# Performance work log

Hardware: AMD Instinct MI355X
Metric: run time of the kernel (lower is better)

The kernel has to match this reference:

```python
import jax, jax.numpy as jnp
import numpy as np

N_NODES = 40000


def gcn_conv(x, W, b, src, dst, deg_inv_sqrt, n_nodes):
    # x: [N, Din], W: [Din, Dout]
    h = x @ W  # [N, Dout]
    norm = deg_inv_sqrt[src] * deg_inv_sqrt[dst]  # [E'] (edges incl. self-loops)
    msg = h[src] * norm[:, None]  # gather + scale: [E', Dout]
    out = jax.ops.segment_sum(msg, dst, num_segments=n_nodes)  # scatter-add
    return out + b


def setup_inputs() -> dict:
    key = jax.random.key(0)
    k1, k2, k3, k4, k5, k6 = jax.random.split(key, 6)
    x = jax.random.normal(k1, (N_NODES, 512), dtype=jnp.float32)
    edge_index = jax.random.randint(k2, (2, 640000), 0, N_NODES, dtype=jnp.int64)
    W1 = jax.random.normal(k3, (512, 256), dtype=jnp.float32) * (1.0 / np.sqrt(512))
    b1 = jax.random.normal(k4, (256,), dtype=jnp.float32) * 0.01
    W2 = jax.random.normal(k5, (256, 47), dtype=jnp.float32) * (1.0 / np.sqrt(256))
    b2 = jax.random.normal(k6, (47,), dtype=jnp.float32) * 0.01
    return {"x": x, "edge_index": edge_index, "W1": W1, "b1": b1, "W2": W2, "b2": b2}


def reference(x, edge_index, W1, b1, W2, b2):
    n = x.shape[0]
    loops = jnp.arange(n, dtype=edge_index.dtype)
    # add self-loops (PyG GCNConv default)
    src = jnp.concatenate([edge_index[0], loops])
    dst = jnp.concatenate([edge_index[1], loops])
    # symmetric normalization: deg over A + I (unit edge weights)
    deg = jax.ops.segment_sum(jnp.ones_like(dst, dtype=x.dtype), dst, num_segments=n)
    deg_inv_sqrt = jnp.where(deg > 0, jax.lax.rsqrt(jnp.maximum(deg, 1e-12)), 0.0)

    h = gcn_conv(x, W1, b1, src, dst, deg_inv_sqrt, n)
    h = jax.nn.relu(h)
    # dropout is identity in eval mode (training=False)
    h = gcn_conv(h, W2, b2, src, dst, deg_inv_sqrt, n)
    return jax.nn.log_softmax(h, axis=1)
```

## Files before the change

kernel.cpp:

```cpp
#include <hip/hip_runtime.h>


typedef _Float16 f16;
typedef _Float16 f16x8 __attribute__((ext_vector_type(8)));
typedef float f32x4 __attribute__((ext_vector_type(4)));

#define N_NODES 40000
#define N_EDGES 640000
#define D_IN 512
#define D_HID 256
#define D_OUT 47
#define D_OUT_PAD 48


__global__ void k_degree(const int* __restrict__ eidx, int* __restrict__ deg) {
    int e = blockIdx.x * blockDim.x + threadIdx.x;
    if (e < N_EDGES) atomicAdd(&deg[eidx[N_EDGES + e]], 1);
}

__global__ __launch_bounds__(1024) void k_scan(const int* __restrict__ deg,
                                               int* __restrict__ rowptr,
                                               float* __restrict__ dinv) {
    __shared__ int wsum[16];
    const int S = 40;
    int t = threadIdx.x;
    int lane = t & 63;
    int wid = t >> 6;
    int base = t * S;
    bool live = (base < N_NODES);

    int v[S];
    int tot = 0;
#pragma unroll
    for (int i = 0; i < S / 4; ++i) {
        int4 q = make_int4(0, 0, 0, 0);
        if (live) q = *(const int4*)(deg + base + i * 4);
        v[i * 4 + 0] = q.x; v[i * 4 + 1] = q.y;
        v[i * 4 + 2] = q.z; v[i * 4 + 3] = q.w;
        tot += q.x + q.y + q.z + q.w;
    }
    int inc = tot;
#pragma unroll
    for (int off = 1; off < 64; off <<= 1) {
        int n = __shfl_up(inc, off);
        if (lane >= off) inc += n;
    }
    if (lane == 63) wsum[wid] = inc;
    __syncthreads();
    if (t < 16) {
        int wv = wsum[t];
        int winc = wv;
#pragma unroll
        for (int off = 1; off < 16; off <<= 1) {
            int n = __shfl_up(winc, off);
            if (t >= off) winc += n;
        }
        wsum[t] = winc - wv;
    }
    __syncthreads();
    int acc = wsum[wid] + (inc - tot);
#pragma unroll
    for (int i = 0; i < S / 4; ++i) {
        int4 r; float4 f;
        r.x = acc; f.x = rsqrtf((float)(v[i * 4 + 0] + 1)); acc += v[i * 4 + 0];
        r.y = acc; f.y = rsqrtf((float)(v[i * 4 + 1] + 1)); acc += v[i * 4 + 1];
        r.z = acc; f.z = rsqrtf((float)(v[i * 4 + 2] + 1)); acc += v[i * 4 + 2];
        r.w = acc; f.w = rsqrtf((float)(v[i * 4 + 3] + 1)); acc += v[i * 4 + 3];
        if (live) {
            *(int4*)(rowptr + base + i * 4) = r;
            *(float4*)(dinv + base + i * 4) = f;
        }
    }
    if (t == 0) rowptr[N_NODES] = N_EDGES;
}

__global__ void k_fill(const int* __restrict__ eidx, const int* __restrict__ rowptr,
                       int* __restrict__ cursor, int* __restrict__ col) {
    int e = blockIdx.x * blockDim.x + threadIdx.x;
    if (e < N_EDGES) {
        int s = eidx[e];
        int d = eidx[N_EDGES + e];
        int pos = atomicAdd(&cursor[d], 1);
        col[rowptr[d] + pos] = s;
    }
}


__global__ void k_pack_w1(const float* __restrict__ W, f16* __restrict__ Wp) {
    int u = blockIdx.x * blockDim.x + threadIdx.x;
    if (u >= 16 * 16 * 64) return;
    int l = u & 63;
    int nf = (u >> 6) & 15;
    int kt = u >> 10;
    int k0 = kt * 32 + (l >> 4) * 8;
    int c = nf * 16 + (l & 15);
    f16x8 o;
#pragma unroll
    for (int j = 0; j < 8; ++j) o[j] = (f16)W[(size_t)(k0 + j) * D_HID + c];
    *(f16x8*)(Wp + (size_t)u * 8) = o;
}

__global__ void k_pack_w2(const float* __restrict__ W, f16* __restrict__ Wp) {
    int u = blockIdx.x * blockDim.x + threadIdx.x;
    if (u >= 8 * 3 * 64) return;
    int l = u & 63;
    int nf = (u / 64) % 3;
    int kt = u / 192;
    int k0 = kt * 32 + (l >> 4) * 8;
    int c = nf * 16 + (l & 15);
    f16x8 o;
#pragma unroll
    for (int j = 0; j < 8; ++j)
        o[j] = (c < D_OUT) ? (f16)W[(size_t)(k0 + j) * D_OUT + c] : (f16)0.0f;
    *(f16x8*)(Wp + (size_t)u * 8) = o;
}


__global__ __launch_bounds__(256) void k_gemm1(const float* __restrict__ X,
                                               const f16* __restrict__ Bp,
                                               f16* __restrict__ C) {
    int wid = threadIdx.x >> 6;
    int lane = threadIdx.x & 63;
    int rowBase = blockIdx.x * 64;
    int nf0 = wid * 4;
    int r_ = lane & 15, q_ = lane >> 4;

    f32x4 acc[4][4];
#pragma unroll
    for (int mi = 0; mi < 4; ++mi)
#pragma unroll
        for (int ni = 0; ni < 4; ++ni) acc[mi][ni] = (f32x4)(0.0f);

    for (int kt = 0; kt < 16; ++kt) {
        int k0 = kt * 32 + q_ * 8;
        f16x8 a[4], b[4];
#pragma unroll
        for (int mi = 0; mi < 4; ++mi) {
            const float4* p = (const float4*)(X + (size_t)(rowBase + mi * 16 + r_) * D_IN + k0);
            float4 lo = p[0], hi = p[1];
            f16x8 t;
            t[0] = (f16)lo.x; t[1] = (f16)lo.y; t[2] = (f16)lo.z; t[3] = (f16)lo.w;
            t[4] = (f16)hi.x; t[5] = (f16)hi.y; t[6] = (f16)hi.z; t[7] = (f16)hi.w;
            a[mi] = t;
        }
#pragma unroll
        for (int ni = 0; ni < 4; ++ni)
            b[ni] = *(const f16x8*)(Bp + ((size_t)(kt * 16 + nf0 + ni) * 64 + lane) * 8);
#pragma unroll
        for (int mi = 0; mi < 4; ++mi)
#pragma unroll
            for (int ni = 0; ni < 4; ++ni)
                acc[mi][ni] = __builtin_amdgcn_mfma_f32_16x16x32_f16(a[mi], b[ni], acc[mi][ni], 0, 0, 0);
    }

    int r0 = (lane >> 4) * 4;
    int c0 = lane & 15;
#pragma unroll
    for (int mi = 0; mi < 4; ++mi)
#pragma unroll
        for (int ni = 0; ni < 4; ++ni)
#pragma unroll
            for (int r = 0; r < 4; ++r) {
                int row = rowBase + mi * 16 + r0 + r;
                C[(size_t)row * D_HID + (nf0 + ni) * 16 + c0] = (f16)acc[mi][ni][r];
            }
}


__global__ __launch_bounds__(256) void k_gemm2(const f16* __restrict__ Ap,
                                               const f16* __restrict__ Bp,
                                               f16* __restrict__ C) {
    int wid = threadIdx.x >> 6;
    int lane = threadIdx.x & 63;
    int rowTile = blockIdx.x * 4 + wid;
    int rowBase = rowTile * 64;
    if (rowBase >= N_NODES) return;

    f32x4 acc[4][3];
#pragma unroll
    for (int mi = 0; mi < 4; ++mi)
#pragma unroll
        for (int ni = 0; ni < 3; ++ni) acc[mi][ni] = (f32x4)(0.0f);

    int m16b = rowTile * 4;
    for (int kt = 0; kt < 8; ++kt) {
        f16x8 a[4], b[3];
#pragma unroll
        for (int mi = 0; mi < 4; ++mi)
            a[mi] = *(const f16x8*)(Ap + ((size_t)((m16b + mi) * 8 + kt) * 64 + lane) * 8);
#pragma unroll
        for (int ni = 0; ni < 3; ++ni)
            b[ni] = *(const f16x8*)(Bp + ((size_t)(kt * 3 + ni) * 64 + lane) * 8);
#pragma unroll
        for (int mi = 0; mi < 4; ++mi)
#pragma unroll
            for (int ni = 0; ni < 3; ++ni)
                acc[mi][ni] = __builtin_amdgcn_mfma_f32_16x16x32_f16(a[mi], b[ni], acc[mi][ni], 0, 0, 0);
    }

    int r0 = (lane >> 4) * 4;
    int c0 = lane & 15;
#pragma unroll
    for (int mi = 0; mi < 4; ++mi)
#pragma unroll
        for (int ni = 0; ni < 3; ++ni)
#pragma unroll
            for (int r = 0; r < 4; ++r) {
                int row = rowBase + mi * 16 + r0 + r;
                C[(size_t)row * D_OUT_PAD + ni * 16 + c0] = (f16)acc[mi][ni][r];
            }
}


__global__ __launch_bounds__(256) void k_agg1(const f16* __restrict__ h1,
                                              const int* __restrict__ rowptr,
                                              const int* __restrict__ col,
                                              const float* __restrict__ dinv,
                                              const float* __restrict__ b1,
                                              f16* __restrict__ hp) {
    int node = blockIdx.x * 4 + (threadIdx.x >> 6);
    int lane = threadIdx.x & 63;
    int half = lane >> 5;
    int hl = lane & 31;
    float di = dinv[node];

    f16x8 selfv = *(const f16x8*)(h1 + (size_t)node * D_HID + hl * 8);

    float a[8];
#pragma unroll
    for (int j = 0; j < 8; ++j) a[j] = 0.0f;

    int e0 = rowptr[node], e1 = rowptr[node + 1];
    for (int base = e0; base < e1; base += 64) {
        int nn = min(64, e1 - base);
        int sidx = 0; float wv = 0.0f;
        if (lane < nn) {
            int s = col[base + lane];
            sidx = s;
            wv = dinv[s] * di;
        }
        int t = half;
        for (; t + 2 < nn; t += 4) {
            int s0 = __shfl(sidx, t), s1 = __shfl(sidx, t + 2);
            float w0 = __shfl(wv, t), w1 = __shfl(wv, t + 2);
            f16x8 u0 = *(const f16x8*)(h1 + (size_t)s0 * D_HID + hl * 8);
            f16x8 u1 = *(const f16x8*)(h1 + (size_t)s1 * D_HID + hl * 8);
#pragma unroll
            for (int j = 0; j < 8; ++j)
                a[j] += (float)u0[j] * w0 + (float)u1[j] * w1;
        }
        if (t < nn) {
            int s0 = __shfl(sidx, t);
            float w0 = __shfl(wv, t);
            f16x8 u0 = *(const f16x8*)(h1 + (size_t)s0 * D_HID + hl * 8);
#pragma unroll
            for (int j = 0; j < 8; ++j) a[j] += (float)u0[j] * w0;
        }
    }

#pragma unroll
    for (int j = 0; j < 8; ++j) a[j] += __shfl_xor(a[j], 32);

    float wself = di * di;
    float4 b_lo = *(const float4*)(b1 + hl * 8);
    float4 b_hi = *(const float4*)(b1 + hl * 8 + 4);
    f16x8 o;
    o[0] = (f16)fmaxf(a[0] + (float)selfv[0] * wself + b_lo.x, 0.0f);
    o[1] = (f16)fmaxf(a[1] + (float)selfv[1] * wself + b_lo.y, 0.0f);
    o[2] = (f16)fmaxf(a[2] + (float)selfv[2] * wself + b_lo.z, 0.0f);
    o[3] = (f16)fmaxf(a[3] + (float)selfv[3] * wself + b_lo.w, 0.0f);
    o[4] = (f16)fmaxf(a[4] + (float)selfv[4] * wself + b_hi.x, 0.0f);
    o[5] = (f16)fmaxf(a[5] + (float)selfv[5] * wself + b_hi.y, 0.0f);
    o[6] = (f16)fmaxf(a[6] + (float)selfv[6] * wself + b_hi.z, 0.0f);
    o[7] = (f16)fmaxf(a[7] + (float)selfv[7] * wself + b_hi.w, 0.0f);

    if (half == 0) {
        size_t idx = ((size_t)(node >> 4) * 8 + (hl >> 2)) * 512 + (hl & 3) * 128 + (node & 15) * 8;
        *(f16x8*)(hp + idx) = o;
    }
}


__global__ __launch_bounds__(256) void k_agg2(const f16* __restrict__ g,
                                              const int* __restrict__ rowptr,
                                              const int* __restrict__ col,
                                              const float* __restrict__ dinv,
                                              const float* __restrict__ b2,
                                              float* __restrict__ out) {
    int node = blockIdx.x * 4 + (threadIdx.x >> 6);
    int lane = threadIdx.x & 63;
    float di = dinv[node];
    bool act = lane < D_OUT_PAD;
    float acc = act ? (float)g[(size_t)node * D_OUT_PAD + lane] * di * di : 0.0f;

    int e0 = rowptr[node], e1 = rowptr[node + 1];
    for (int base = e0; base < e1; base += 64) {
        int nn = min(64, e1 - base);
        int sidx = 0; float wv = 0.0f;
        if (lane < nn) {
            int s = col[base + lane];
            sidx = s;
            wv = dinv[s] * di;
        }
        int k = 0;
        for (; k + 4 <= nn; k += 4) {
            int s0 = __shfl(sidx, k), s1 = __shfl(sidx, k + 1);
            int s2 = __shfl(sidx, k + 2), s3 = __shfl(sidx, k + 3);
            float w0 = __shfl(wv, k), w1 = __shfl(wv, k + 1);
            float w2 = __shfl(wv, k + 2), w3 = __shfl(wv, k + 3);
            if (act) {
                float u0 = (float)g[(size_t)s0 * D_OUT_PAD + lane];
                float u1 = (float)g[(size_t)s1 * D_OUT_PAD + lane];
                float u2 = (float)g[(size_t)s2 * D_OUT_PAD + lane];
                float u3 = (float)g[(size_t)s3 * D_OUT_PAD + lane];
                acc += u0 * w0 + u1 * w1 + u2 * w2 + u3 * w3;
            }
        }
        for (; k < nn; ++k) {
            int s0 = __shfl(sidx, k);
            float w0 = __shfl(wv, k);
            if (act) acc += (float)g[(size_t)s0 * D_OUT_PAD + lane] * w0;
        }
    }

    float z = (lane < D_OUT) ? acc + b2[lane] : -3.0e38f;
    float mx = z;
#pragma unroll
    for (int off = 32; off >= 1; off >>= 1) mx = fmaxf(mx, __shfl_xor(mx, off));
    float ex = (lane < D_OUT) ? expf(z - mx) : 0.0f;
    float sum = ex;
#pragma unroll
    for (int off = 32; off >= 1; off >>= 1) sum += __shfl_xor(sum, off);
    if (lane < D_OUT) out[(size_t)node * D_OUT + lane] = z - mx - logf(sum);
}


extern "C" void kernel_launch(void* const* d_in, const int* in_sizes, int n_in,
                              void* d_out, int out_size, void* d_ws, size_t ws_size,
                              hipStream_t stream) {
    const float* x  = (const float*)d_in[0];
    const int*   ei = (const int*)d_in[1];
    const float* W1 = (const float*)d_in[2];
    const float* b1 = (const float*)d_in[3];
    const float* W2 = (const float*)d_in[4];
    const float* b2 = (const float*)d_in[5];
    float* out = (float*)d_out;

    char* ws = (char*)d_ws;
    int*   degi   = (int*)(ws + 0);
    int*   cursor = (int*)(ws + 160000);
    float* dinv   = (float*)(ws + 320000);
    int*   rowptr = (int*)(ws + 480000);
    int*   col    = (int*)(ws + 640256);
    f16*   w1p    = (f16*)(ws + 3200256);
    f16*   w2p    = (f16*)(ws + 3462400);
    f16*   h1     = (f16*)(ws + 3486976);
    f16*   hpk    = (f16*)(ws + 23966976);
    f16*   g      = (f16*)(ws + 44446976);

    hipMemsetAsync(d_ws, 0, 320000, stream);

    k_degree<<<2500, 256, 0, stream>>>(ei, degi);
    k_scan<<<1, 1024, 0, stream>>>(degi, rowptr, dinv);
    k_fill<<<2500, 256, 0, stream>>>(ei, rowptr, cursor, col);

    k_pack_w1<<<64, 256, 0, stream>>>(W1, w1p);
    k_pack_w2<<<6, 256, 0, stream>>>(W2, w2p);

    k_gemm1<<<625, 256, 0, stream>>>(x, w1p, h1);
    k_agg1<<<10000, 256, 0, stream>>>(h1, rowptr, col, dinv, b1, hpk);
    k_gemm2<<<157, 256, 0, stream>>>(hpk, w2p, g);
    k_agg2<<<10000, 256, 0, stream>>>(g, rowptr, col, dinv, b2, out);
}
```

Baseline: 224.9 us.

## Retile gemm1 to 32x64 warp tiles with double-buffered register prefetch

Each block of gemm1 now covers a 64-row by 128-column tile instead of 64 rows by 256 columns, and each warp owns 32 rows by 64 columns. The grid doubles to 1250 blocks. The k-loop is fully unrolled with two register sets, so loads for the next k-step are issued before the MFMAs of the current step to hide global-load latency. The cost is that every X row is now read twice from global (once per column half) and register pressure goes up from the double buffering.

```diff
diff --git a/kernel.cpp b/kernel.cpp
--- a/kernel.cpp
+++ b/kernel.cpp
@@ -116,53 +116,86 @@
 }
 
 
+#define G1_LOADA(areg, kt_)                                                  \
+    {                                                                        \
+        int k0 = (kt_) * 32 + q_ * 8;                                        \
+        const float4* p0 = (const float4*)(xrow0 + k0);                      \
+        const float4* p1 = (const float4*)(xrow1 + k0);                      \
+        float4 lo0 = p0[0], hi0 = p0[1], lo1 = p1[0], hi1 = p1[1];           \
+        f16x8 t0, t1;                                                        \
+        t0[0] = (f16)lo0.x; t0[1] = (f16)lo0.y; t0[2] = (f16)lo0.z;          \
+        t0[3] = (f16)lo0.w; t0[4] = (f16)hi0.x; t0[5] = (f16)hi0.y;          \
+        t0[6] = (f16)hi0.z; t0[7] = (f16)hi0.w;                              \
+        t1[0] = (f16)lo1.x; t1[1] = (f16)lo1.y; t1[2] = (f16)lo1.z;          \
+        t1[3] = (f16)lo1.w; t1[4] = (f16)hi1.x; t1[5] = (f16)hi1.y;          \
+        t1[6] = (f16)hi1.z; t1[7] = (f16)hi1.w;                              \
+        areg##0 = t0; areg##1 = t1;                                          \
+    }
+
+#define G1_LOADB(breg, kt_)                                                  \
+    {                                                                        \
+        const f16* bp = Bp + ((size_t)((kt_) * 16 + nf0) * 64 + lane) * 8;   \
+        breg##0 = *(const f16x8*)(bp);                                       \
+        breg##1 = *(const f16x8*)(bp + 512);                                 \
+        breg##2 = *(const f16x8*)(bp + 1024);                                \
+        breg##3 = *(const f16x8*)(bp + 1536);                                \
+    }
+
+#define G1_MFMA(areg, breg)                                                  \
+    acc00 = __builtin_amdgcn_mfma_f32_16x16x32_f16(areg##0, breg##0, acc00, 0, 0, 0); \
+    acc01 = __builtin_amdgcn_mfma_f32_16x16x32_f16(areg##0, breg##1, acc01, 0, 0, 0); \
+    acc02 = __builtin_amdgcn_mfma_f32_16x16x32_f16(areg##0, breg##2, acc02, 0, 0, 0); \
+    acc03 = __builtin_amdgcn_mfma_f32_16x16x32_f16(areg##0, breg##3, acc03, 0, 0, 0); \
+    acc10 = __builtin_amdgcn_mfma_f32_16x16x32_f16(areg##1, breg##0, acc10, 0, 0, 0); \
+    acc11 = __builtin_amdgcn_mfma_f32_16x16x32_f16(areg##1, breg##1, acc11, 0, 0, 0); \
+    acc12 = __builtin_amdgcn_mfma_f32_16x16x32_f16(areg##1, breg##2, acc12, 0, 0, 0); \
+    acc13 = __builtin_amdgcn_mfma_f32_16x16x32_f16(areg##1, breg##3, acc13, 0, 0, 0);
+
 __global__ __launch_bounds__(256) void k_gemm1(const float* __restrict__ X,
                                                const f16* __restrict__ Bp,
                                                f16* __restrict__ C) {
     int wid = threadIdx.x >> 6;
     int lane = threadIdx.x & 63;
-    int rowBase = blockIdx.x * 64;
-    int nf0 = wid * 4;
+    int rb = blockIdx.x >> 1;
+    int cb = blockIdx.x & 1;
+    int rowBase = rb * 64 + (wid >> 1) * 32;
+    int nf0 = cb * 8 + (wid & 1) * 4;
     int r_ = lane & 15, q_ = lane >> 4;
 
-    f32x4 acc[4][4];
-#pragma unroll
-    for (int mi = 0; mi < 4; ++mi)
-#pragma unroll
-        for (int ni = 0; ni < 4; ++ni) acc[mi][ni] = (f32x4)(0.0f);
-
-    for (int kt = 0; kt < 16; ++kt) {
-        int k0 = kt * 32 + q_ * 8;
-        f16x8 a[4], b[4];
-#pragma unroll
-        for (int mi = 0; mi < 4; ++mi) {
-            const float4* p = (const float4*)(X + (size_t)(rowBase + mi * 16 + r_) * D_IN + k0);
-            float4 lo = p[0], hi = p[1];
-            f16x8 t;
-            t[0] = (f16)lo.x; t[1] = (f16)lo.y; t[2] = (f16)lo.z; t[3] = (f16)lo.w;
-            t[4] = (f16)hi.x; t[5] = (f16)hi.y; t[6] = (f16)hi.z; t[7] = (f16)hi.w;
-            a[mi] = t;
-        }
-#pragma unroll
-        for (int ni = 0; ni < 4; ++ni)
-            b[ni] = *(const f16x8*)(Bp + ((size_t)(kt * 16 + nf0 + ni) * 64 + lane) * 8);
-#pragma unroll
-        for (int mi = 0; mi < 4; ++mi)
-#pragma unroll
-            for (int ni = 0; ni < 4; ++ni)
-                acc[mi][ni] = __builtin_amdgcn_mfma_f32_16x16x32_f16(a[mi], b[ni], acc[mi][ni], 0, 0, 0);
+    const float* xrow0 = X + (size_t)(rowBase + r_) * D_IN;
+    const float* xrow1 = X + (size_t)(rowBase + 16 + r_) * D_IN;
+
+    f32x4 acc00 = (f32x4)(0.0f), acc01 = (f32x4)(0.0f), acc02 = (f32x4)(0.0f), acc03 = (f32x4)(0.0f);
+    f32x4 acc10 = (f32x4)(0.0f), acc11 = (f32x4)(0.0f), acc12 = (f32x4)(0.0f), acc13 = (f32x4)(0.0f);
+
+    f16x8 pA0, pA1, pB0, pB1, pB2, pB3;
+    f16x8 qA0, qA1, qB0, qB1, qB2, qB3;
+
+    G1_LOADA(pA, 0)
+    G1_LOADB(pB, 0)
+#pragma unroll
+    for (int kt = 0; kt < 16; kt += 2) {
+        G1_LOADA(qA, kt + 1)
+        G1_LOADB(qB, kt + 1)
+        G1_MFMA(pA, pB)
+        if (kt + 2 < 16) {
+            G1_LOADA(pA, kt + 2)
+            G1_LOADB(pB, kt + 2)
+        }
+        G1_MFMA(qA, qB)
     }
 
     int r0 = (lane >> 4) * 4;
     int c0 = lane & 15;
-#pragma unroll
-    for (int mi = 0; mi < 4; ++mi)
+    f32x4 accs[2][4] = {{acc00, acc01, acc02, acc03}, {acc10, acc11, acc12, acc13}};
+#pragma unroll
+    for (int mi = 0; mi < 2; ++mi)
 #pragma unroll
         for (int ni = 0; ni < 4; ++ni)
 #pragma unroll
             for (int r = 0; r < 4; ++r) {
                 int row = rowBase + mi * 16 + r0 + r;
-                C[(size_t)row * D_HID + (nf0 + ni) * 16 + c0] = (f16)acc[mi][ni][r];
+                C[(size_t)row * D_HID + (nf0 + ni) * 16 + c0] = (f16)accs[mi][ni][r];
             }
 }
 
@@ -367,7 +400,7 @@
     k_pack_w1<<<64, 256, 0, stream>>>(W1, w1p);
     k_pack_w2<<<6, 256, 0, stream>>>(W2, w2p);
 
-    k_gemm1<<<625, 256, 0, stream>>>(x, w1p, h1);
+    k_gemm1<<<1250, 256, 0, stream>>>(x, w1p, h1);
     k_agg1<<<10000, 256, 0, stream>>>(h1, rowptr, col, dinv, b1, hpk);
     k_gemm2<<<157, 256, 0, stream>>>(hpk, w2p, g);
     k_agg2<<<10000, 256, 0, stream>>>(g, rowptr, col, dinv, b2, out);
```

Result: no change. 221.8 us (-1.3%).

## Stage converted X tile in LDS and split GEMM1 across eight waves

Applied to the files above, without the earlier changes.

GEMM1 now loads the block's 64x512 fp32 X tile once with coalesced float4 reads, converts it to fp16 and stores it in padded shared memory. The MFMA loop then reads A fragments from LDS. Block size goes from 4 to 8 waves, with each wave covering 2 output column tiles instead of 4, so the X rows are not read redundantly by every wave from global memory. In exchange it uses about 66 KB of LDS per block, which limits how many blocks fit per CU, and adds a full-tile sync before any compute starts.

```diff
diff --git a/kernel.cpp b/kernel.cpp
--- a/kernel.cpp
+++ b/kernel.cpp
@@ -3,6 +3,7 @@
 
 typedef _Float16 f16;
 typedef _Float16 f16x8 __attribute__((ext_vector_type(8)));
+typedef _Float16 f16x4 __attribute__((ext_vector_type(4)));
 typedef float f32x4 __attribute__((ext_vector_type(4)));
 
 #define N_NODES 40000
@@ -116,49 +117,58 @@
 }
 
 
-__global__ __launch_bounds__(256) void k_gemm1(const float* __restrict__ X,
+__global__ __launch_bounds__(512) void k_gemm1(const float* __restrict__ X,
                                                const f16* __restrict__ Bp,
                                                f16* __restrict__ C) {
-    int wid = threadIdx.x >> 6;
-    int lane = threadIdx.x & 63;
+    __shared__ f16 As[64][520];
+    int t = threadIdx.x;
+    int lane = t & 63;
+    int wid = t >> 6;
     int rowBase = blockIdx.x * 64;
-    int nf0 = wid * 4;
+
+#pragma unroll
+    for (int it = 0; it < 16; ++it) {
+        int idx = it * 512 + t;
+        int row = idx >> 7;
+        int c4 = idx & 127;
+        float4 v = *(const float4*)(X + (size_t)(rowBase + row) * D_IN + c4 * 4);
+        f16x4 o;
+        o[0] = (f16)v.x; o[1] = (f16)v.y; o[2] = (f16)v.z; o[3] = (f16)v.w;
+        *(f16x4*)(&As[row][c4 * 4]) = o;
+    }
+    __syncthreads();
+
+    int nf0 = wid * 2;
     int r_ = lane & 15, q_ = lane >> 4;
 
-    f32x4 acc[4][4];
+    f32x4 acc[4][2];
 #pragma unroll
     for (int mi = 0; mi < 4; ++mi)
 #pragma unroll
-        for (int ni = 0; ni < 4; ++ni) acc[mi][ni] = (f32x4)(0.0f);
-
+        for (int ni = 0; ni < 2; ++ni) acc[mi][ni] = (f32x4)(0.0f);
+
+#pragma unroll 4
     for (int kt = 0; kt < 16; ++kt) {
-        int k0 = kt * 32 + q_ * 8;
-        f16x8 a[4], b[4];
-#pragma unroll
-        for (int mi = 0; mi < 4; ++mi) {
-            const float4* p = (const float4*)(X + (size_t)(rowBase + mi * 16 + r_) * D_IN + k0);
-            float4 lo = p[0], hi = p[1];
-            f16x8 t;
-            t[0] = (f16)lo.x; t[1] = (f16)lo.y; t[2] = (f16)lo.z; t[3] = (f16)lo.w;
-            t[4] = (f16)hi.x; t[5] = (f16)hi.y; t[6] = (f16)hi.z; t[7] = (f16)hi.w;
-            a[mi] = t;
-        }
-#pragma unroll
-        for (int ni = 0; ni < 4; ++ni)
+        f16x8 a[4], b[2];
+#pragma unroll
+        for (int mi = 0; mi < 4; ++mi)
+            a[mi] = *(const f16x8*)(&As[mi * 16 + r_][kt * 32 + q_ * 8]);
+#pragma unroll
+        for (int ni = 0; ni < 2; ++ni)
             b[ni] = *(const f16x8*)(Bp + ((size_t)(kt * 16 + nf0 + ni) * 64 + lane) * 8);
 #pragma unroll
         for (int mi = 0; mi < 4; ++mi)
 #pragma unroll
-            for (int ni = 0; ni < 4; ++ni)
+            for (int ni = 0; ni < 2; ++ni)
                 acc[mi][ni] = __builtin_amdgcn_mfma_f32_16x16x32_f16(a[mi], b[ni], acc[mi][ni], 0, 0, 0);
     }
 
-    int r0 = (lane >> 4) * 4;
-    int c0 = lane & 15;
+    int r0 = q_ * 4;
+    int c0 = r_;
 #pragma unroll
     for (int mi = 0; mi < 4; ++mi)
 #pragma unroll
-        for (int ni = 0; ni < 4; ++ni)
+        for (int ni = 0; ni < 2; ++ni)
 #pragma unroll
             for (int r = 0; r < 4; ++r) {
                 int row = rowBase + mi * 16 + r0 + r;
@@ -367,7 +377,7 @@
     k_pack_w1<<<64, 256, 0, stream>>>(W1, w1p);
     k_pack_w2<<<6, 256, 0, stream>>>(W2, w2p);
 
-    k_gemm1<<<625, 256, 0, stream>>>(x, w1p, h1);
+    k_gemm1<<<625, 512, 0, stream>>>(x, w1p, h1);
     k_agg1<<<10000, 256, 0, stream>>>(h1, rowptr, col, dinv, b1, hpk);
     k_gemm2<<<157, 256, 0, stream>>>(hpk, w2p, g);
     k_agg2<<<10000, 256, 0, stream>>>(g, rowptr, col, dinv, b2, out);
```

Measured after the change: 199.0 us. 1.13x faster.
